# Kernel tuning notes

Hardware: AMD Instinct MI355X
Metric: run time of the kernel (lower is better)

The kernel has to match this reference:

```python
import jax, jax.numpy as jnp
import numpy as np

NT = 30
T = 60
STATES = NT + T
N = 48
NEG = -1e9


def setup_inputs() -> dict:
    key = jax.random.key(0)
    k1, k2, k3 = jax.random.split(key, 3)
    unary_scores = jax.random.normal(k1, (N, T), dtype=jnp.float32)
    rule_scores = jax.random.normal(k2, (NT, STATES, STATES), dtype=jnp.float32)
    root_scores = jax.random.normal(k3, (NT,), dtype=jnp.float32)
    return {"unary_scores": unary_scores, "rule_scores": rule_scores, "root_scores": root_scores}


def reference(unary_scores, rule_scores, root_scores):
    # CKY inside algorithm in the log semiring (PCFGVMap._inside).
    n, t_states = unary_scores.shape
    nt = rule_scores.shape[0]
    states = nt + t_states
    # alpha[i, j, A]: inside score of span (i, j) headed by state A.
    alpha = jnp.full((n, n, states), NEG, dtype=unary_scores.dtype)
    diag = jnp.arange(n)
    # Terminal spans: only preterminal slots [nt:] are filled; NT slots stay at NEG,
    # which contributes exactly 0 after exp in the stable logsumexp below, so using
    # the full `states` range reproduces the original's sliced (T-only / NT-only) math.
    alpha = alpha.at[diag, diag, nt:].set(unary_scores)

    for l in range(1, n):  # span length (static unroll over the n-1 CKY diagonals)
        s = jnp.arange(n - l)          # span start i; span is (i, i+l)
        m = jnp.arange(l)              # split offsets: k = i + m
        left = alpha[s[:, None], s[:, None] + m[None, :], :]            # [spans, splits, S]
        right = alpha[s[:, None] + m[None, :] + 1, s[:, None] + l, :]   # [spans, splits, S]
        # scores[s, m, A, B, C] = left[s,m,B] + right[s,m,C] + rule[A,B,C]
        scores = (left[:, :, None, :, None]
                  + right[:, :, None, None, :]
                  + rule_scores[None, None, :, :, :])
        new = jax.nn.logsumexp(scores, axis=(1, 3, 4))                  # [spans, nt]
        alpha = alpha.at[s, s + l, :nt].set(new)

    log_Z = jax.nn.logsumexp(alpha[0, n - 1, :nt] + root_scores)
    return log_Z
```

## Files before the change

kernel.cpp:

```cpp
#include <hip/hip_runtime.h>
#include <math.h>

#define NT 30
#define TT 60
#define S  90
#define NN 48
#define SS (S*S)
#define PB 72

typedef __attribute__((ext_vector_type(8))) short bf16x8;
typedef __attribute__((ext_vector_type(4))) float f32x4;

__device__ __forceinline__ unsigned ordKey(float f) {
    unsigned u = __float_as_uint(f);
    return (u & 0x80000000u) ? ~u : (u | 0x80000000u);
}
__device__ __forceinline__ float decKey(unsigned k) {
    unsigned u = (k & 0x80000000u) ? (k ^ 0x80000000u) : ~k;
    return __uint_as_float(u);
}
__device__ __forceinline__ unsigned short f2bf(float f) {
    unsigned u = __float_as_uint(f);
    return (unsigned short)((u + 0x7fffu + ((u >> 16) & 1u)) >> 16);
}
__device__ __forceinline__ float bf2f(unsigned short h) {
    return __uint_as_float(((unsigned)h) << 16);
}

__global__ void k_prep(const float* __restrict__ rule, const float* __restrict__ unary,
                       unsigned short* __restrict__ eruleB, unsigned short* __restrict__ svec,
                       float* __restrict__ scal, unsigned* __restrict__ mkey) {
    const int b    = blockIdx.x;
    const int lane = threadIdx.x;
    if (b < 1080) {
        const int a = b / 36, tIdx = b - a * 36;
        const int bt = tIdx / 6, ct = tIdx - bt * 6;
        ushort4 vv;
        unsigned short* pv = (unsigned short*)&vv;
#pragma unroll
        for (int reg = 0; reg < 4; ++reg) {
            int bb = bt * 16 + (lane >> 4) * 4 + reg;
            int cc = ct * 16 + (lane & 15);
            float val = (bb < S && cc < S) ? __expf(rule[a * SS + bb * S + cc]) : 0.f;
            pv[reg] = f2bf(val);
        }
        *(ushort4*)(eruleB + ((a * 36 + tIdx) * 64 + lane) * 4) = vv;
    } else {
        const int i = b - 1080;
        float u = (lane < TT) ? unary[i * TT + lane] : -INFINITY;
        float m = u;
        for (int o = 32; o > 0; o >>= 1) m = fmaxf(m, __shfl_down(m, o));
        m = __shfl(m, 0);
        for (int t = lane; t < 96; t += 64)
            svec[(i * NN + i) * 96 + t] =
                (t >= NT && t < S) ? f2bf(__expf(unary[i * TT + (t - NT)] - m)) : (unsigned short)0;
        if (lane == 0) scal[i * NN + i] = m;
        if (lane < NN) mkey[i * NN + lane] = (lane == i) ? ordKey(m) : 0u;
    }
}

__global__ __launch_bounds__(384, 1) void k_level(int l,
                                                  const unsigned short* __restrict__ eruleB,
                                                  unsigned short* __restrict__ svec,
                                                  float* __restrict__ scal,
                                                  unsigned* __restrict__ mkey) {
    const int s0   = blockIdx.x;
    const int a    = blockIdx.y;
    const int j    = s0 + l;
    const int cell = s0 * NN + j;
    const int tid  = threadIdx.x;
    const int lane = tid & 63;
    const int w    = tid >> 6;

    __shared__ unsigned short elT[96 * PB];
    __shared__ unsigned short erT[96 * PB];
    __shared__ float fL[48], fR[48];
    __shared__ float part[6];
    __shared__ float Msh;

    uint2 rv[6];
    {
        const unsigned short* rp = eruleB + (a * 36 + w * 6) * 256 + lane * 4;
#pragma unroll
        for (int tc = 0; tc < 6; ++tc) rv[tc] = *(const uint2*)(rp + tc * 256);
    }

    if (w == 0) {
        float msum = -INFINITY, sl = 0.f, sr = 0.f, mrv = 0.f;
        if (lane < l) {
            int cl = s0 * NN + s0 + lane;
            int cr = (s0 + lane + 1) * NN + j;
            float mlv = decKey(mkey[cl]);
            mrv = decKey(mkey[cr]);
            sl = scal[cl]; sr = scal[cr];
            msum = mlv + mrv;
        }
        float v = msum;
        for (int o = 32; o > 0; o >>= 1) v = fmaxf(v, __shfl_down(v, o));
        float M = __shfl(v, 0);
        if (lane == 0) Msh = M;
        if (lane < l) {
            fL[lane] = __expf(sl + mrv - M);
            fR[lane] = __expf(sr - mrv);
        }
    }
    __syncthreads();

    const int K = (l > 32) ? 64 : 32;
    const unsigned short* lb = svec + (s0 * NN + s0) * 96;
    for (int i = tid; i < 96 * K; i += 384) {
        int r = i / 96, x = i - r * 96;
        float vl = 0.f, vr = 0.f;
        if (r < l) {
            vl = bf2f(lb[r * 96 + x]) * fL[r];
            vr = bf2f(svec[((s0 + r + 1) * NN + j) * 96 + x]) * fR[r];
        }
        elT[x * PB + r] = f2bf(vl);
        erT[x * PB + r] = f2bf(vr);
    }
    __syncthreads();

    f32x4 acc[6];
    {
        f32x4 zz = {0.f, 0.f, 0.f, 0.f};
#pragma unroll
        for (int tc = 0; tc < 6; ++tc) acc[tc] = zz;
    }
    const int arow = w * 16 + (lane & 15);
    const int koff = (lane >> 4) * 8;
    for (int ks = 0; ks < (K >> 5); ++ks) {
        bf16x8 af = *(const bf16x8*)(elT + arow * PB + ks * 32 + koff);
#pragma unroll
        for (int tc = 0; tc < 6; ++tc) {
            bf16x8 bfr = *(const bf16x8*)(erT + (tc * 16 + (lane & 15)) * PB + ks * 32 + koff);
            acc[tc] = __builtin_amdgcn_mfma_f32_16x16x32_bf16(af, bfr, acc[tc], 0, 0, 0);
        }
    }

    float p = 0.f;
#pragma unroll
    for (int tc = 0; tc < 6; ++tc) {
        float r0 = __uint_as_float((rv[tc].x & 0xffffu) << 16);
        float r1 = __uint_as_float(rv[tc].x & 0xffff0000u);
        float r2 = __uint_as_float((rv[tc].y & 0xffffu) << 16);
        float r3 = __uint_as_float(rv[tc].y & 0xffff0000u);
        p += r0 * acc[tc][0] + r1 * acc[tc][1]
           + r2 * acc[tc][2] + r3 * acc[tc][3];
    }
    for (int o = 32; o > 0; o >>= 1) p += __shfl_down(p, o);
    if (lane == 0) part[w] = p;
    __syncthreads();

    if (a == 0 && tid >= NT && tid < 96) svec[cell * 96 + tid] = 0;
    if (tid == 0) {
        float sum = part[0] + part[1] + part[2] + part[3] + part[4] + part[5];
        float alpha = Msh + logf(sum);
        svec[cell * 96 + a] = f2bf(sum);
        if (a == 0) scal[cell] = Msh;
        atomicMax(&mkey[cell], ordKey(alpha));
    }
}

__global__ void k_final(const float* __restrict__ root, const unsigned short* __restrict__ svec,
                        const float* __restrict__ scal, float* __restrict__ out) {
    const int t = threadIdx.x;
    const int cell = NN - 1;
    float v = (t < NT) ? scal[cell] + logf(bf2f(svec[cell * 96 + t])) + root[t] : -INFINITY;
    float m = v;
    for (int o = 32; o > 0; o >>= 1) m = fmaxf(m, __shfl_down(m, o));
    m = __shfl(m, 0);
    float e = (t < NT) ? __expf(v - m) : 0.f;
    for (int o = 32; o > 0; o >>= 1) e += __shfl_down(e, o);
    if (t == 0) out[0] = m + logf(e);
}

extern "C" void kernel_launch(void* const* d_in, const int* in_sizes, int n_in,
                              void* d_out, int out_size, void* d_ws, size_t ws_size,
                              hipStream_t stream) {
    const float* unary = (const float*)d_in[0];
    const float* rule  = (const float*)d_in[1];
    const float* root  = (const float*)d_in[2];
    float* out = (float*)d_out;

    float*          ws     = (float*)d_ws;
    unsigned short* eruleB = (unsigned short*)ws;
    unsigned short* svec   = eruleB + 30 * 36 * 256;
    float*          scal   = (float*)(svec + NN * NN * 96);
    unsigned*       mkey   = (unsigned*)(scal + NN * NN);

    k_prep<<<1128, 64, 0, stream>>>(rule, unary, eruleB, svec, scal, mkey);
    for (int l = 1; l < NN; ++l) {
        k_level<<<dim3(NN - l, 30), 384, 0, stream>>>(l, eruleB, svec, scal, mkey);
    }
    k_final<<<1, 64, 0, stream>>>(root, svec, scal, out);
}
```

Before: 322.0 us.

## Fuse two CKY span levels per launch and compute all NT heads per block

Each launch now handles two consecutive span lengths. Blocks for the longer span recompute the two needed shorter-span child cells locally in shared memory rather than waiting for a separate launch, which halves the number of kernel launches. Each block now also computes all 30 nonterminal outputs from one shared MFMA accumulator rather than one block per nonterminal. That removes the atomicMax ordered-key scheme in favour of a per-cell max written directly. The cost is fewer blocks per launch (no 30x grid), serial per-block loops over 30 rule slices, and redundant recomputation of two cells for the level-B blocks.

```diff
diff --git a/kernel.cpp b/kernel.cpp
--- a/kernel.cpp
+++ b/kernel.cpp
@@ -11,14 +11,6 @@
 typedef __attribute__((ext_vector_type(8))) short bf16x8;
 typedef __attribute__((ext_vector_type(4))) float f32x4;
 
-__device__ __forceinline__ unsigned ordKey(float f) {
-    unsigned u = __float_as_uint(f);
-    return (u & 0x80000000u) ? ~u : (u | 0x80000000u);
-}
-__device__ __forceinline__ float decKey(unsigned k) {
-    unsigned u = (k & 0x80000000u) ? (k ^ 0x80000000u) : ~k;
-    return __uint_as_float(u);
-}
 __device__ __forceinline__ unsigned short f2bf(float f) {
     unsigned u = __float_as_uint(f);
     return (unsigned short)((u + 0x7fffu + ((u >> 16) & 1u)) >> 16);
@@ -27,9 +19,130 @@
     return __uint_as_float(((unsigned)h) << 16);
 }
 
+struct CellLds {
+    unsigned short elT[96 * PB];
+    unsigned short erT[96 * PB];
+    float fL[48], fR[48];
+    float part[NT][6];
+    float alph[NT];
+    unsigned short svL[96], svR[96], svO[96];
+    float resL[2], resR[2], resO[2];
+};
+
+__device__ void cellCompute(int s0, int j, int l,
+                            const unsigned short* __restrict__ eruleB,
+                            const unsigned short* __restrict__ svec,
+                            const float* __restrict__ scal,
+                            const float* __restrict__ mlog,
+                            int rL, const unsigned short* ovL, float scalL, float mlogL,
+                            int rR, const unsigned short* ovR, float scalR, float mlogR,
+                            CellLds& L, unsigned short* outSv, float* outRes) {
+    const int tid  = threadIdx.x;
+    const int lane = tid & 63;
+    const int w    = tid >> 6;
+
+    if (w == 0) {
+        float msum = -INFINITY, sl = 0.f, sr = 0.f, mrv = 0.f;
+        if (lane < l) {
+            int cl = s0 * NN + s0 + lane;
+            int cr = (s0 + lane + 1) * NN + j;
+            float mlv = (lane == rL) ? mlogL : mlog[cl];
+            mrv       = (lane == rR) ? mlogR : mlog[cr];
+            sl        = (lane == rL) ? scalL : scal[cl];
+            sr        = (lane == rR) ? scalR : scal[cr];
+            msum = mlv + mrv;
+        }
+        float v = msum;
+        for (int o = 32; o > 0; o >>= 1) v = fmaxf(v, __shfl_down(v, o));
+        float M = __shfl(v, 0);
+        if (lane == 0) outRes[0] = M;
+        if (lane < l) {
+            L.fL[lane] = __expf(sl + mrv - M);
+            L.fR[lane] = __expf(sr - mrv);
+        }
+    }
+    {
+        uint4 z = {0u, 0u, 0u, 0u};
+        uint4* z1 = (uint4*)L.elT;
+        uint4* z2 = (uint4*)L.erT;
+        for (int i = tid; i < 96 * PB / 8; i += 384) { z1[i] = z; z2[i] = z; }
+    }
+    __syncthreads();
+
+    for (int i = tid; i < l * 24; i += 384) {
+        int r = i / 24, x0 = (i - r * 24) * 4;
+        const unsigned short* pl = (r == rL) ? (ovL + x0)
+                                             : (svec + (s0 * NN + s0 + r) * 96 + x0);
+        const unsigned short* pr = (r == rR) ? (ovR + x0)
+                                             : (svec + ((s0 + r + 1) * NN + j) * 96 + x0);
+        ushort4 a4 = *(const ushort4*)pl;
+        ushort4 b4 = *(const ushort4*)pr;
+        float fl = L.fL[r], fr = L.fR[r];
+        unsigned short* eld = L.elT + x0 * PB + r;
+        unsigned short* erd = L.erT + x0 * PB + r;
+        eld[0 * PB] = f2bf(bf2f(a4.x) * fl); eld[1 * PB] = f2bf(bf2f(a4.y) * fl);
+        eld[2 * PB] = f2bf(bf2f(a4.z) * fl); eld[3 * PB] = f2bf(bf2f(a4.w) * fl);
+        erd[0 * PB] = f2bf(bf2f(b4.x) * fr); erd[1 * PB] = f2bf(bf2f(b4.y) * fr);
+        erd[2 * PB] = f2bf(bf2f(b4.z) * fr); erd[3 * PB] = f2bf(bf2f(b4.w) * fr);
+    }
+    __syncthreads();
+
+    const int K = (l > 32) ? 64 : 32;
+    f32x4 acc[6];
+    {
+        f32x4 zz = {0.f, 0.f, 0.f, 0.f};
+#pragma unroll
+        for (int tc = 0; tc < 6; ++tc) acc[tc] = zz;
+    }
+    const int arow = w * 16 + (lane & 15);
+    const int koff = (lane >> 4) * 8;
+    for (int ks = 0; ks < (K >> 5); ++ks) {
+        bf16x8 af = *(const bf16x8*)(L.elT + arow * PB + ks * 32 + koff);
+#pragma unroll
+        for (int tc = 0; tc < 6; ++tc) {
+            bf16x8 bfr = *(const bf16x8*)(L.erT + (tc * 16 + (lane & 15)) * PB + ks * 32 + koff);
+            acc[tc] = __builtin_amdgcn_mfma_f32_16x16x32_bf16(af, bfr, acc[tc], 0, 0, 0);
+        }
+    }
+
+#pragma unroll 2
+    for (int a = 0; a < NT; ++a) {
+        const unsigned short* rp = eruleB + (a * 36 + w * 6) * 256 + lane * 4;
+        float p = 0.f;
+#pragma unroll
+        for (int tc = 0; tc < 6; ++tc) {
+            uint2 rv = *(const uint2*)(rp + tc * 256);
+            float r0 = __uint_as_float((rv.x & 0xffffu) << 16);
+            float r1 = __uint_as_float(rv.x & 0xffff0000u);
+            float r2 = __uint_as_float((rv.y & 0xffffu) << 16);
+            float r3 = __uint_as_float(rv.y & 0xffff0000u);
+            p += r0 * acc[tc][0] + r1 * acc[tc][1]
+               + r2 * acc[tc][2] + r3 * acc[tc][3];
+        }
+        for (int o = 32; o > 0; o >>= 1) p += __shfl_down(p, o);
+        if (lane == 0) L.part[a][w] = p;
+    }
+    __syncthreads();
+
+    if (tid < NT) {
+        float s = L.part[tid][0] + L.part[tid][1] + L.part[tid][2]
+                + L.part[tid][3] + L.part[tid][4] + L.part[tid][5];
+        L.alph[tid] = s;
+        outSv[tid] = f2bf(s);
+    }
+    if (tid >= NT && tid < 96) outSv[tid] = 0;
+    __syncthreads();
+    if (w == 0) {
+        float s = (lane < NT) ? L.alph[lane] : -INFINITY;
+        for (int o = 32; o > 0; o >>= 1) s = fmaxf(s, __shfl_down(s, o));
+        if (lane == 0) outRes[1] = outRes[0] + logf(s);
+    }
+    __syncthreads();
+}
+
 __global__ void k_prep(const float* __restrict__ rule, const float* __restrict__ unary,
                        unsigned short* __restrict__ eruleB, unsigned short* __restrict__ svec,
-                       float* __restrict__ scal, unsigned* __restrict__ mkey) {
+                       float* __restrict__ scal, float* __restrict__ mlog) {
     const int b    = blockIdx.x;
     const int lane = threadIdx.x;
     if (b < 1080) {
@@ -54,111 +167,45 @@
         for (int t = lane; t < 96; t += 64)
             svec[(i * NN + i) * 96 + t] =
                 (t >= NT && t < S) ? f2bf(__expf(unary[i * TT + (t - NT)] - m)) : (unsigned short)0;
-        if (lane == 0) scal[i * NN + i] = m;
-        if (lane < NN) mkey[i * NN + lane] = (lane == i) ? ordKey(m) : 0u;
-    }
-}
-
-__global__ __launch_bounds__(384, 1) void k_level(int l,
-                                                  const unsigned short* __restrict__ eruleB,
-                                                  unsigned short* __restrict__ svec,
-                                                  float* __restrict__ scal,
-                                                  unsigned* __restrict__ mkey) {
-    const int s0   = blockIdx.x;
-    const int a    = blockIdx.y;
-    const int j    = s0 + l;
-    const int cell = s0 * NN + j;
-    const int tid  = threadIdx.x;
-    const int lane = tid & 63;
-    const int w    = tid >> 6;
-
-    __shared__ unsigned short elT[96 * PB];
-    __shared__ unsigned short erT[96 * PB];
-    __shared__ float fL[48], fR[48];
-    __shared__ float part[6];
-    __shared__ float Msh;
-
-    uint2 rv[6];
-    {
-        const unsigned short* rp = eruleB + (a * 36 + w * 6) * 256 + lane * 4;
-#pragma unroll
-        for (int tc = 0; tc < 6; ++tc) rv[tc] = *(const uint2*)(rp + tc * 256);
-    }
-
-    if (w == 0) {
-        float msum = -INFINITY, sl = 0.f, sr = 0.f, mrv = 0.f;
-        if (lane < l) {
-            int cl = s0 * NN + s0 + lane;
-            int cr = (s0 + lane + 1) * NN + j;
-            float mlv = decKey(mkey[cl]);
-            mrv = decKey(mkey[cr]);
-            sl = scal[cl]; sr = scal[cr];
-            msum = mlv + mrv;
-        }
-        float v = msum;
-        for (int o = 32; o > 0; o >>= 1) v = fmaxf(v, __shfl_down(v, o));
-        float M = __shfl(v, 0);
-        if (lane == 0) Msh = M;
-        if (lane < l) {
-            fL[lane] = __expf(sl + mrv - M);
-            fR[lane] = __expf(sr - mrv);
-        }
-    }
-    __syncthreads();
-
-    const int K = (l > 32) ? 64 : 32;
-    const unsigned short* lb = svec + (s0 * NN + s0) * 96;
-    for (int i = tid; i < 96 * K; i += 384) {
-        int r = i / 96, x = i - r * 96;
-        float vl = 0.f, vr = 0.f;
-        if (r < l) {
-            vl = bf2f(lb[r * 96 + x]) * fL[r];
-            vr = bf2f(svec[((s0 + r + 1) * NN + j) * 96 + x]) * fR[r];
-        }
-        elT[x * PB + r] = f2bf(vl);
-        erT[x * PB + r] = f2bf(vr);
-    }
-    __syncthreads();
-
-    f32x4 acc[6];
-    {
-        f32x4 zz = {0.f, 0.f, 0.f, 0.f};
-#pragma unroll
-        for (int tc = 0; tc < 6; ++tc) acc[tc] = zz;
-    }
-    const int arow = w * 16 + (lane & 15);
-    const int koff = (lane >> 4) * 8;
-    for (int ks = 0; ks < (K >> 5); ++ks) {
-        bf16x8 af = *(const bf16x8*)(elT + arow * PB + ks * 32 + koff);
-#pragma unroll
-        for (int tc = 0; tc < 6; ++tc) {
-            bf16x8 bfr = *(const bf16x8*)(erT + (tc * 16 + (lane & 15)) * PB + ks * 32 + koff);
-            acc[tc] = __builtin_amdgcn_mfma_f32_16x16x32_bf16(af, bfr, acc[tc], 0, 0, 0);
-        }
-    }
-
-    float p = 0.f;
-#pragma unroll
-    for (int tc = 0; tc < 6; ++tc) {
-        float r0 = __uint_as_float((rv[tc].x & 0xffffu) << 16);
-        float r1 = __uint_as_float(rv[tc].x & 0xffff0000u);
-        float r2 = __uint_as_float((rv[tc].y & 0xffffu) << 16);
-        float r3 = __uint_as_float(rv[tc].y & 0xffff0000u);
-        p += r0 * acc[tc][0] + r1 * acc[tc][1]
-           + r2 * acc[tc][2] + r3 * acc[tc][3];
-    }
-    for (int o = 32; o > 0; o >>= 1) p += __shfl_down(p, o);
-    if (lane == 0) part[w] = p;
-    __syncthreads();
-
-    if (a == 0 && tid >= NT && tid < 96) svec[cell * 96 + tid] = 0;
-    if (tid == 0) {
-        float sum = part[0] + part[1] + part[2] + part[3] + part[4] + part[5];
-        float alpha = Msh + logf(sum);
-        svec[cell * 96 + a] = f2bf(sum);
-        if (a == 0) scal[cell] = Msh;
-        atomicMax(&mkey[cell], ordKey(alpha));
-    }
+        if (lane == 0) { scal[i * NN + i] = m; mlog[i * NN + i] = m; }
+    }
+}
+
+__global__ __launch_bounds__(384, 1) void k_pair(int lA,
+                                                 const unsigned short* __restrict__ eruleB,
+                                                 unsigned short* __restrict__ svec,
+                                                 float* __restrict__ scal,
+                                                 float* __restrict__ mlog) {
+    __shared__ CellLds L;
+    const int tid = threadIdx.x;
+    const int nA  = NN - lA;
+
+    int cell;
+    if ((int)blockIdx.x < nA) {
+        const int s0 = blockIdx.x;
+        const int j  = s0 + lA;
+        cell = s0 * NN + j;
+        cellCompute(s0, j, lA, eruleB, svec, scal, mlog,
+                    -1, nullptr, 0.f, 0.f, -1, nullptr, 0.f, 0.f,
+                    L, L.svO, L.resO);
+    } else {
+        const int s0 = blockIdx.x - nA;
+        const int lB = lA + 1;
+        const int j  = s0 + lB;
+        cell = s0 * NN + j;
+        cellCompute(s0, s0 + lA, lA, eruleB, svec, scal, mlog,
+                    -1, nullptr, 0.f, 0.f, -1, nullptr, 0.f, 0.f,
+                    L, L.svL, L.resL);
+        cellCompute(s0 + 1, s0 + 1 + lA, lA, eruleB, svec, scal, mlog,
+                    -1, nullptr, 0.f, 0.f, -1, nullptr, 0.f, 0.f,
+                    L, L.svR, L.resR);
+        cellCompute(s0, j, lB, eruleB, svec, scal, mlog,
+                    lA, L.svL, L.resL[0], L.resL[1],
+                    0,  L.svR, L.resR[0], L.resR[1],
+                    L, L.svO, L.resO);
+    }
+    if (tid < 96) svec[cell * 96 + tid] = L.svO[tid];
+    if (tid == 0) { scal[cell] = L.resO[0]; mlog[cell] = L.resO[1]; }
 }
 
 __global__ void k_final(const float* __restrict__ root, const unsigned short* __restrict__ svec,
@@ -186,11 +233,13 @@
     unsigned short* eruleB = (unsigned short*)ws;
     unsigned short* svec   = eruleB + 30 * 36 * 256;
     float*          scal   = (float*)(svec + NN * NN * 96);
-    unsigned*       mkey   = (unsigned*)(scal + NN * NN);
-
-    k_prep<<<1128, 64, 0, stream>>>(rule, unary, eruleB, svec, scal, mkey);
-    for (int l = 1; l < NN; ++l) {
-        k_level<<<dim3(NN - l, 30), 384, 0, stream>>>(l, eruleB, svec, scal, mkey);
+    float*          mlog   = scal + NN * NN;
+
+    k_prep<<<1128, 64, 0, stream>>>(rule, unary, eruleB, svec, scal, mlog);
+    for (int lA = 1; lA < NN; lA += 2) {
+        int nA = NN - lA;
+        int nB = (lA + 1 < NN) ? NN - (lA + 1) : 0;
+        k_pair<<<nA + nB, 384, 0, stream>>>(lA, eruleB, svec, scal, mlog);
     }
     k_final<<<1, 64, 0, stream>>>(root, svec, scal, out);
 }
```

After: 1.166 ms. 262% more time.

## Fuse final logsumexp into last level, zero svec upfront, vectorize staging

Applied to the files above, without the earlier changes.

Removes the separate k_final launch by having the last-level blocks accumulate exp(root)-weighted sums atomically, with the last-arriving block writing the output. The NT-slot zeroing of svec moves from every level kernel into k_prep. The LDS staging now zero-fills the tiles once and writes four split rows per thread as ushort4, touching only the ceil(l/4) groups needed instead of all K rows. This trades one kernel launch and the scalar staging stores for atomics and a threadfence in the final level.

```diff
diff --git a/kernel.cpp b/kernel.cpp
--- a/kernel.cpp
+++ b/kernel.cpp
@@ -29,9 +29,19 @@
 
 __global__ void k_prep(const float* __restrict__ rule, const float* __restrict__ unary,
                        unsigned short* __restrict__ eruleB, unsigned short* __restrict__ svec,
-                       float* __restrict__ scal, unsigned* __restrict__ mkey) {
+                       float* __restrict__ scal, unsigned* __restrict__ mkey,
+                       float* __restrict__ facc, unsigned* __restrict__ fdone) {
     const int b    = blockIdx.x;
     const int lane = threadIdx.x;
+
+    unsigned* usv = (unsigned*)svec;
+    for (int u = b * 64 + lane; u < NN * NN * 48; u += 1128 * 64) {
+        int cellIdx = u / 48;
+        int i = cellIdx / NN, jj = cellIdx - i * NN;
+        if (i != jj) usv[u] = 0u;
+    }
+    if (b == 0 && lane == 0) { facc[0] = 0.f; fdone[0] = 0u; }
+
     if (b < 1080) {
         const int a = b / 36, tIdx = b - a * 36;
         const int bt = tIdx / 6, ct = tIdx - bt * 6;
@@ -63,7 +73,11 @@
                                                   const unsigned short* __restrict__ eruleB,
                                                   unsigned short* __restrict__ svec,
                                                   float* __restrict__ scal,
-                                                  unsigned* __restrict__ mkey) {
+                                                  unsigned* __restrict__ mkey,
+                                                  const float* __restrict__ root,
+                                                  float* __restrict__ facc,
+                                                  unsigned* __restrict__ fdone,
+                                                  float* __restrict__ out) {
     const int s0   = blockIdx.x;
     const int a    = blockIdx.y;
     const int j    = s0 + l;
@@ -74,7 +88,7 @@
 
     __shared__ unsigned short elT[96 * PB];
     __shared__ unsigned short erT[96 * PB];
-    __shared__ float fL[48], fR[48];
+    __shared__ float fLs[48], fRs[48];
     __shared__ float part[6];
     __shared__ float Msh;
 
@@ -100,26 +114,38 @@
         float M = __shfl(v, 0);
         if (lane == 0) Msh = M;
         if (lane < l) {
-            fL[lane] = __expf(sl + mrv - M);
-            fR[lane] = __expf(sr - mrv);
-        }
+            fLs[lane] = __expf(sl + mrv - M);
+            fRs[lane] = __expf(sr - mrv);
+        }
+    } else {
+        uint4 z = {0u, 0u, 0u, 0u};
+        uint4* z1 = (uint4*)elT;
+        uint4* z2 = (uint4*)erT;
+        for (int i = tid - 64; i < 96 * PB / 8; i += 320) { z1[i] = z; z2[i] = z; }
     }
     __syncthreads();
 
+    const int gmax = (l + 3) >> 2;
+    for (int i = tid; i < gmax * S; i += 384) {
+        int g = i / S, x = i - g * S;
+        int r0 = g * 4;
+        const unsigned short* pl = svec + (s0 * NN + s0 + r0) * 96 + x;
+        const unsigned short* pr = svec + ((s0 + r0 + 1) * NN + j) * 96 + x;
+        ushort4 lv, rv4;
+        unsigned short* plv = (unsigned short*)&lv;
+        unsigned short* prv = (unsigned short*)&rv4;
+#pragma unroll
+        for (int k = 0; k < 4; ++k) {
+            int r = r0 + k;
+            plv[k] = (r < l) ? f2bf(bf2f(pl[k * 96]) * fLs[r]) : (unsigned short)0;
+            prv[k] = (r < l) ? f2bf(bf2f(pr[k * (NN * 96)]) * fRs[r]) : (unsigned short)0;
+        }
+        *(ushort4*)(elT + x * PB + r0) = lv;
+        *(ushort4*)(erT + x * PB + r0) = rv4;
+    }
+    __syncthreads();
+
     const int K = (l > 32) ? 64 : 32;
-    const unsigned short* lb = svec + (s0 * NN + s0) * 96;
-    for (int i = tid; i < 96 * K; i += 384) {
-        int r = i / 96, x = i - r * 96;
-        float vl = 0.f, vr = 0.f;
-        if (r < l) {
-            vl = bf2f(lb[r * 96 + x]) * fL[r];
-            vr = bf2f(svec[((s0 + r + 1) * NN + j) * 96 + x]) * fR[r];
-        }
-        elT[x * PB + r] = f2bf(vl);
-        erT[x * PB + r] = f2bf(vr);
-    }
-    __syncthreads();
-
     f32x4 acc[6];
     {
         f32x4 zz = {0.f, 0.f, 0.f, 0.f};
@@ -151,27 +177,20 @@
     if (lane == 0) part[w] = p;
     __syncthreads();
 
-    if (a == 0 && tid >= NT && tid < 96) svec[cell * 96 + tid] = 0;
     if (tid == 0) {
         float sum = part[0] + part[1] + part[2] + part[3] + part[4] + part[5];
-        float alpha = Msh + logf(sum);
-        svec[cell * 96 + a] = f2bf(sum);
-        if (a == 0) scal[cell] = Msh;
-        atomicMax(&mkey[cell], ordKey(alpha));
-    }
-}
-
-__global__ void k_final(const float* __restrict__ root, const unsigned short* __restrict__ svec,
-                        const float* __restrict__ scal, float* __restrict__ out) {
-    const int t = threadIdx.x;
-    const int cell = NN - 1;
-    float v = (t < NT) ? scal[cell] + logf(bf2f(svec[cell * 96 + t])) + root[t] : -INFINITY;
-    float m = v;
-    for (int o = 32; o > 0; o >>= 1) m = fmaxf(m, __shfl_down(m, o));
-    m = __shfl(m, 0);
-    float e = (t < NT) ? __expf(v - m) : 0.f;
-    for (int o = 32; o > 0; o >>= 1) e += __shfl_down(e, o);
-    if (t == 0) out[0] = m + logf(e);
+        if (l == NN - 1) {
+            atomicAdd(facc, sum * __expf(root[a]));
+            __threadfence();
+            unsigned old = atomicAdd(fdone, 1u);
+            if (old == 29u) out[0] = Msh + logf(atomicAdd(facc, 0.0f));
+        } else {
+            float alpha = Msh + logf(sum);
+            svec[cell * 96 + a] = f2bf(sum);
+            if (a == 0) scal[cell] = Msh;
+            atomicMax(&mkey[cell], ordKey(alpha));
+        }
+    }
 }
 
 extern "C" void kernel_launch(void* const* d_in, const int* in_sizes, int n_in,
@@ -187,10 +206,12 @@
     unsigned short* svec   = eruleB + 30 * 36 * 256;
     float*          scal   = (float*)(svec + NN * NN * 96);
     unsigned*       mkey   = (unsigned*)(scal + NN * NN);
-
-    k_prep<<<1128, 64, 0, stream>>>(rule, unary, eruleB, svec, scal, mkey);
+    float*          facc   = (float*)(mkey + NN * NN);
+    unsigned*       fdone  = (unsigned*)(facc + 1);
+
+    k_prep<<<1128, 64, 0, stream>>>(rule, unary, eruleB, svec, scal, mkey, facc, fdone);
     for (int l = 1; l < NN; ++l) {
-        k_level<<<dim3(NN - l, 30), 384, 0, stream>>>(l, eruleB, svec, scal, mkey);
-    }
-    k_final<<<1, 64, 0, stream>>>(root, svec, scal, out);
-}
+        k_level<<<dim3(NN - l, 30), 384, 0, stream>>>(l, eruleB, svec, scal, mkey,
+                                                      root, facc, fdone, out);
+    }
+}
```

New measurement: 300.2 us. 6.8% less time.
